# Kernel tuning notes

Hardware: AMD Instinct MI355X
Metric: run time of the kernel (lower is better)

## Reference

```python
import jax, jax.numpy as jnp
from jax import lax
import numpy as np

B, T, TW, EW = 32, 64, 32, 300   # dialogues, utterances, words, word-embed
H = 512                          # lstm hidden per direction
E = 2 * H                        # utterance embedding size
HH = 512                         # emotion hidden size
C = 7                            # output classes


def setup_inputs() -> dict:
    key = jax.random.key(0)
    ks = jax.random.split(key, 24)
    n = lambda k, shp: (jax.random.normal(k, shp, dtype=jnp.float32) * 0.05)
    inp = {
        "input_data": jax.random.normal(ks[0], (B, T, TW, EW), dtype=jnp.float32),
        # BiLSTM (torch gate order i,f,g,o)
        "lstm_Wih_f": n(ks[1], (4 * H, EW)), "lstm_Whh_f": n(ks[2], (4 * H, H)), "lstm_b_f": n(ks[3], (4 * H,)),
        "lstm_Wih_b": n(ks[4], (4 * H, EW)), "lstm_Whh_b": n(ks[5], (4 * H, H)), "lstm_b_b": n(ks[6], (4 * H,)),
        # attention weight
        "W_att": n(ks[7], (E, E)),
        # global-state GRUCell (torch gate order r,z,n)
        "g_Wih": n(ks[8], (3 * E, E)), "g_Whh": n(ks[9], (3 * E, E)), "g_bih": n(ks[10], (3 * E,)), "g_bhh": n(ks[11], (3 * E,)),
        # party-state GRUCell
        "p_Wih": n(ks[12], (3 * E, E)), "p_Whh": n(ks[13], (3 * E, E)), "p_bih": n(ks[14], (3 * E,)), "p_bhh": n(ks[15], (3 * E,)),
        # emotion-state GRUCell (input E, hidden HH)
        "e_Wih": n(ks[16], (3 * HH, E)), "e_Whh": n(ks[17], (3 * HH, HH)), "e_bih": n(ks[18], (3 * HH,)), "e_bhh": n(ks[19], (3 * HH,)),
        # classifier
        "cls_W": n(ks[20], (C, HH)), "cls_b": n(ks[21], (C,)),
    }
    return inp


def _gru_cell(x, h, Wih, Whh, bih, bhh):
    gi = x @ Wih.T + bih
    gh = h @ Whh.T + bhh
    ir, iz, inn = jnp.split(gi, 3, axis=-1)
    hr, hz, hn = jnp.split(gh, 3, axis=-1)
    r = jax.nn.sigmoid(ir + hr)
    z = jax.nn.sigmoid(iz + hz)
    n = jnp.tanh(inn + r * hn)
    return (1.0 - z) * n + z * h


def _lstm_last_hidden(xs, Wih, Whh, b):
    # xs: [Tw, N, Ew] -> final hidden [N, H]
    N = xs.shape[1]
    h0 = jnp.zeros((N, H), xs.dtype)

    def step(carry, x):
        h, c = carry
        g = x @ Wih.T + h @ Whh.T + b
        i_, f_, g_, o_ = jnp.split(g, 4, axis=-1)
        c2 = jax.nn.sigmoid(f_) * c + jax.nn.sigmoid(i_) * jnp.tanh(g_)
        h2 = jax.nn.sigmoid(o_) * jnp.tanh(c2)
        return (h2, c2), None

    (h, _), _ = lax.scan(step, (h0, h0), xs)
    return h


def _forward(input_data, lstm_Wih_f, lstm_Whh_f, lstm_b_f, lstm_Wih_b, lstm_Whh_b, lstm_b_b,
             W_att, g_Wih, g_Whh, g_bih, g_bhh, p_Wih, p_Whh, p_bih, p_bhh,
             e_Wih, e_Whh, e_bih, e_bhh, cls_W, cls_b):
    # ---- FeatureExtraction: BiLSTM over words, take fwd-last + bwd-first hidden ----
    x = input_data.reshape(B * T, TW, EW).transpose(1, 0, 2)          # [Tw, N, Ew]
    h_fwd = _lstm_last_hidden(x, lstm_Wih_f, lstm_Whh_f, lstm_b_f)     # [N, H]
    h_bwd = _lstm_last_hidden(x[::-1], lstm_Wih_b, lstm_Whh_b, lstm_b_b)  # [N, H]
    feats = jnp.concatenate([h_fwd, h_bwd], axis=-1).reshape(B, T, E)  # [B, T, 2H]

    # ---- EmotionDetection: sequential recurrence over utterances ----
    utt = feats.transpose(1, 0, 2)                                     # [T, B, E]
    hist0 = jnp.zeros((T + 1, B, E), feats.dtype)   # global_state history (idx 0 = zero init)
    party0 = jnp.zeros((2, B, E), feats.dtype)
    emo0 = jnp.zeros((B, HH), feats.dtype)
    l_idx = jnp.arange(T + 1)[:, None]              # [T+1, 1]

    def step(carry, inp):
        hist, party, emo = carry
        x_i, i = inp
        p = i % 2
        g_prev = hist[i]                                               # global_state[i]
        new_g = _gru_cell(x_i + party[p], g_prev, g_Wih, g_Whh, g_bih, g_bhh)
        hist = hist.at[i + 1].set(new_g)
        # attention over history indices 0..i (excludes the just-appended state)
        q = x_i @ W_att                                                # [B, E]
        scores = jnp.einsum('be,lbe->lb', q, hist)                     # [T+1, B]
        scores = jnp.where(l_idx <= i, scores, -jnp.inf)
        w = jax.nn.softmax(scores, axis=0)[:, :, None]                 # [T+1, B, 1]
        context = jnp.sum(hist * w, axis=0)                            # [B, E]
        new_p = _gru_cell(x_i + context, party[p], p_Wih, p_Whh, p_bih, p_bhh)
        party = party.at[p].set(new_p)
        emo = _gru_cell(new_p, emo, e_Wih, e_Whh, e_bih, e_bhh)        # [B, HH]
        return (hist, party, emo), emo

    _, emo_seq = lax.scan(step, (hist0, party0, emo0), (utt, jnp.arange(T)))
    emo_seq = emo_seq.transpose(1, 0, 2)                               # [B, T, HH]
    return emo_seq @ cls_W.T + cls_b                                   # [B, T, C]


def reference(input_data, lstm_Wih_f, lstm_Whh_f, lstm_b_f, lstm_Wih_b, lstm_Whh_b, lstm_b_b,
              W_att, g_Wih, g_Whh, g_bih, g_bhh, p_Wih, p_Whh, p_bih, p_bhh,
              e_Wih, e_Whh, e_bih, e_bhh, cls_W, cls_b):
    return _forward(input_data, lstm_Wih_f, lstm_Whh_f, lstm_b_f, lstm_Wih_b, lstm_Whh_b, lstm_b_b,
                    W_att, g_Wih, g_Whh, g_bih, g_bhh, p_Wih, p_Whh, p_bih, p_bhh,
                    e_Wih, e_Whh, e_bih, e_bhh, cls_W, cls_b)
```

## Files before the change

kernel.cpp:

```cpp
#include <hip/hip_runtime.h>
#include <math.h>

#define B_  32
#define T_  64
#define TW_ 32
#define EW_ 300
#define H_  512
#define E_  1024
#define HH_ 512
#define C_  7
#define N_  2048

typedef float f32x4 __attribute__((ext_vector_type(4)));
typedef short s16x8 __attribute__((ext_vector_type(8)));
typedef unsigned short u16;
typedef unsigned int u32;

__device__ __forceinline__ float sigm(float x){ return 1.f/(1.f+expf(-x)); }
__device__ __forceinline__ float bf2f(u16 u){
  union{float f; unsigned v;} x; x.v = ((unsigned)u)<<16; return x.f;
}
__device__ __forceinline__ u16 f2bf(float f){
  union{float f; unsigned v;} x; x.f = f;
  unsigned r = x.v + 0x7FFF + ((x.v>>16)&1);
  return (u16)(r>>16);
}
__device__ __forceinline__ void g2lds16(const void* g, void* l){
  __builtin_amdgcn_global_load_lds((const __attribute__((address_space(1))) u32*)g,
                                   (__attribute__((address_space(3))) u32*)l, 16, 0, 0);
}

__global__ __launch_bounds__(256) void k_pack_w(
    const float* __restrict__ Wih_f, const float* __restrict__ Whh_f,
    const float* __restrict__ Wih_b, const float* __restrict__ Whh_b,
    u16* __restrict__ Wpk)
{
  size_t idx = (size_t)blockIdx.x*256 + threadIdx.x;
  if(idx >= (size_t)32*26*4096) return;
  int c   = (int)(idx & 31);
  int row = (int)((idx >> 5) & 127);
  int kc  = (int)((idx >> 12) % 26);
  int pan = (int)(idx / ((size_t)26*4096));
  int dir = pan >> 4, mt = pan & 15;
  int g = row >> 5, ml = row & 31;
  int R = g*512 + mt*32 + ml;
  int k = kc*32 + c;
  const float* Wih = dir ? Wih_b : Wih_f;
  const float* Whh = dir ? Whh_b : Whh_f;
  float v = (k < 320) ? ((k < EW_) ? Wih[(size_t)R*EW_ + k] : 0.f)
                      : Whh[(size_t)R*H_ + (k-320)];
  Wpk[idx] = f2bf(v);
}

__global__ __launch_bounds__(256) void k_pack_x(
    const float* __restrict__ input, u16* __restrict__ xpk)
{
  size_t idx = (size_t)blockIdx.x*256 + threadIdx.x;
  if(idx >= (size_t)32*32*10*2048) return;
  int c   = (int)(idx & 31);
  int row = (int)((idx >> 5) & 63);
  int kc  = (int)((idx >> 11) % 10);
  int q2  = (int)((idx >> 11) / 10);
  int nt  = q2 & 31, wt = q2 >> 5;
  int n = nt*64 + row;
  int k = kc*32 + c;
  float v = (k < EW_) ? input[((size_t)n*TW_ + wt)*EW_ + k] : 0.f;
  xpk[idx] = f2bf(v);
}

__global__ __launch_bounds__(256) void k_f2bf(const float* __restrict__ src,
                                              u16* __restrict__ dst, int n)
{
  int idx = blockIdx.x*256 + threadIdx.x;
  if(idx < n) dst[idx] = f2bf(src[idx]);
}

__global__ __launch_bounds__(256) void k_wattT(const float* __restrict__ W,
                                               u16* __restrict__ dst)
{
  int idx = blockIdx.x*256 + threadIdx.x;
  if(idx >= E_*E_) return;
  int j = idx >> 10, k = idx & 1023;
  dst[idx] = f2bf(W[(size_t)k*E_ + j]);
}

__global__ __launch_bounds__(256, 4) void lstm4(
    const u16* __restrict__ xpk, const u16* __restrict__ Wpk,
    const float* __restrict__ b_f, const float* __restrict__ b_b,
    const u16* __restrict__ hpk_in, u16* __restrict__ hpk_out,
    float* __restrict__ cb, u16* __restrict__ featsbf, int t)
{
  const int panel = blockIdx.x, nt = blockIdx.y;
  const int dir = panel & 1, mt = panel >> 1;
  const int wt = dir ? (TW_-1-t) : t;
  const u16* srcW = Wpk + (size_t)(dir*16+mt)*26*4096;
  const u16* srcX = xpk + (size_t)(wt*32+nt)*10*2048;
  const u16* srcH = hpk_in + (size_t)(dir*32+nt)*16*2048;

  __shared__ __align__(16) u16 As[3][2048];
  __shared__ __align__(16) u16 Bs[3][4096];

  const int tid = threadIdx.x;
  const int w = tid >> 6, l = tid & 63;
  const int lr = l & 15, lh = l >> 4;
  const int wn = w >> 1, wm = w & 1;

  f32x4 acc[2][4];
  #pragma unroll
  for(int a=0;a<2;a++)
    #pragma unroll
    for(int g=0;g<4;g++) acc[a][g] = (f32x4){0.f,0.f,0.f,0.f};

  auto stage = [&](int kc, int b){
    const u16* aB = (kc < 10) ? (srcX + (size_t)kc*2048) : (srcH + (size_t)(kc-10)*2048);
    const u16* bB = srcW + (size_t)kc*4096;
    g2lds16((const char*)aB + w*1024 + l*16,       (char*)&As[b][0] + w*1024);
    g2lds16((const char*)bB + (w*2)*1024 + l*16,   (char*)&Bs[b][0] + (w*2)*1024);
    g2lds16((const char*)bB + (w*2+1)*1024 + l*16, (char*)&Bs[b][0] + (w*2+1)*1024);
  };

  stage(0, 0);
  stage(1, 1);
  #pragma unroll
  for(int kc=0; kc<26; ++kc){
    if(kc < 25) asm volatile("s_waitcnt vmcnt(3)" ::: "memory");
    else        asm volatile("s_waitcnt vmcnt(0)" ::: "memory");
    __builtin_amdgcn_s_barrier();
    __builtin_amdgcn_sched_barrier(0);
    if(kc+2 < 26) stage(kc+2, (kc+2)%3);
    const int cu = kc % 3;
    s16x8 av[2], bv[4];
    #pragma unroll
    for(int nf=0; nf<2; ++nf)
      av[nf] = *(const s16x8*)&As[cu][(wn*32 + nf*16 + lr)*32 + lh*8];
    #pragma unroll
    for(int g=0; g<4; ++g)
      bv[g] = *(const s16x8*)&Bs[cu][(g*32 + wm*16 + lr)*32 + lh*8];
    #pragma unroll
    for(int g=0; g<4; ++g)
      #pragma unroll
      for(int nf=0; nf<2; ++nf)
        acc[nf][g] = __builtin_amdgcn_mfma_f32_16x16x32_bf16(av[nf], bv[g], acc[nf][g], 0,0,0);
  }

  const float* bias = dir ? b_b : b_f;
  const int col = wm*16 + lr;
  const int m = mt*32 + col;
  const float bi = bias[m], bfv = bias[H_+m], bg = bias[2*H_+m], bo = bias[3*H_+m];
  float* cbp = cb + (size_t)dir*N_*H_;
  u16* hop = hpk_out + ((size_t)(dir*32+nt)*16 + mt)*2048;
  const int n0 = nt*64;
  #pragma unroll
  for(int nf=0; nf<2; ++nf){
    #pragma unroll
    for(int r=0; r<4; ++r){
      const int row = wn*32 + nf*16 + lh*4 + r;
      const int n = n0 + row;
      float gi = acc[nf][0][r] + bi;
      float gf = acc[nf][1][r] + bfv;
      float gc = acc[nf][2][r] + bg;
      float go = acc[nf][3][r] + bo;
      float c_old = cbp[(size_t)n*H_ + m];
      float c2 = sigm(gf)*c_old + sigm(gi)*tanhf(gc);
      float h2 = sigm(go)*tanhf(c2);
      cbp[(size_t)n*H_ + m] = c2;
      if(t == TW_-1) featsbf[(size_t)n*E_ + dir*H_ + m] = f2bf(h2);
      else           hop[row*32 + col] = f2bf(h2);
    }
  }
}

__global__ __launch_bounds__(256) void k_qgemm(const u16* __restrict__ featsbf,
                                               const u16* __restrict__ WattT,
                                               float* __restrict__ q)
{
  const int n0 = blockIdx.x*64, j0 = blockIdx.y*64;
  __shared__ __align__(16) u16 As[64*40];
  __shared__ __align__(16) u16 Bs[64*40];
  const int tid = threadIdx.x;
  const int w = tid>>6, l = tid&63, lr = l&15, lk = (l>>4)*8;
  const int arow = tid>>2, ak8 = (tid&3)*8;

  f32x4 acc[4];
  #pragma unroll
  for(int i=0;i<4;i++) acc[i] = (f32x4){0.f,0.f,0.f,0.f};

  for(int kc=0; kc<32; ++kc){
    *(s16x8*)&As[arow*40 + ak8] = *(const s16x8*)&featsbf[(size_t)(n0+arow)*E_ + kc*32 + ak8];
    *(s16x8*)&Bs[arow*40 + ak8] = *(const s16x8*)&WattT[(size_t)(j0+arow)*E_ + kc*32 + ak8];
    __syncthreads();
    s16x8 av = *(const s16x8*)&As[(w*16 + lr)*40 + lk];
    #pragma unroll
    for(int mf=0; mf<4; ++mf){
      s16x8 bv = *(const s16x8*)&Bs[(mf*16 + lr)*40 + lk];
      acc[mf] = __builtin_amdgcn_mfma_f32_16x16x32_bf16(av, bv, acc[mf], 0,0,0);
    }
    __syncthreads();
  }
  #pragma unroll
  for(int mf=0; mf<4; ++mf)
    #pragma unroll
    for(int r=0; r<4; ++r){
      int n = n0 + w*16 + (l>>4)*4 + r;
      q[(size_t)n*E_ + j0 + mf*16 + lr] = acc[mf][r];
    }
}

struct GArg2 {
  const u16* xA; const u16* xB;
  long ldA; long ldB;
  const u16* W; int K;
};

__device__ __forceinline__ void gemm32v2(const GArg2 a, int R, int xt, int ks,
                                         int KS, int z, float* __restrict__ part,
                                         char* smem)
{
  u16* Xs0 = (u16*)smem;
  u16* Xs1 = Xs0 + 32*40;
  u16* Ws0 = Xs1 + 32*40;
  u16* Ws1 = Ws0 + 128*32;
  const int Kc = a.K / KS;
  const int nch = Kc >> 5;
  const int kb0 = ks * Kc;
  const int tid = threadIdx.x;
  const int w = tid>>6, l = tid&63, lr = l&15, lh = l>>4;

  f32x4 a00={0,0,0,0}, a01={0,0,0,0}, a10={0,0,0,0}, a11={0,0,0,0};

  auto issueW = [&](int c, u16* Wb){
    const int kb = kb0 + c*32;
    #pragma unroll
    for(int c2=0;c2<2;++c2){
      const int cc = w*2 + c2;
      const char* g = (const char*)(a.W + (size_t)(xt*128 + cc*16 + (l>>2))*a.K + kb) + (l&3)*16;
      g2lds16(g, (char*)Wb + cc*1024);
    }
  };
  auto loadX = [&](int c, short4* xr){
    const int kb = kb0 + c*32;
    const int row = tid>>3, k4 = (tid&7)*4;
    short4 xv = *(const short4*)&a.xA[(size_t)row*a.ldA + kb + k4];
    if(a.xB){
      short4 yv = *(const short4*)&a.xB[(size_t)row*a.ldB + kb + k4];
      xv.x = (short)f2bf(bf2f((u16)xv.x)+bf2f((u16)yv.x));
      xv.y = (short)f2bf(bf2f((u16)xv.y)+bf2f((u16)yv.y));
      xv.z = (short)f2bf(bf2f((u16)xv.z)+bf2f((u16)yv.z));
      xv.w = (short)f2bf(bf2f((u16)xv.w)+bf2f((u16)yv.w));
    }
    *xr = xv;
  };
  auto writeX = [&](short4 xv, u16* Xb){
    *(short4*)&Xb[(tid>>3)*40 + (tid&7)*4] = xv;
  };

  short4 xr;
  issueW(0, Ws0); loadX(0, &xr); writeX(xr, Xs0);
  __syncthreads();
  for(int c=0;c<nch;++c){
    u16* Xc = (c&1)?Xs1:Xs0; u16* Wc = (c&1)?Ws1:Ws0;
    u16* Xn = (c&1)?Xs0:Xs1; u16* Wn = (c&1)?Ws0:Ws1;
    const bool pre = (c+1 < nch);
    if(pre){ issueW(c+1, Wn); loadX(c+1, &xr); }
    s16x8 av0 = *(const s16x8*)&Xc[lr*40 + lh*8];
    s16x8 av1 = *(const s16x8*)&Xc[(16+lr)*40 + lh*8];
    s16x8 bv0 = *(const s16x8*)&Wc[(w*32 + lr)*32 + lh*8];
    s16x8 bv1 = *(const s16x8*)&Wc[(w*32 + 16 + lr)*32 + lh*8];
    a00 = __builtin_amdgcn_mfma_f32_16x16x32_bf16(av0, bv0, a00, 0,0,0);
    a01 = __builtin_amdgcn_mfma_f32_16x16x32_bf16(av0, bv1, a01, 0,0,0);
    a10 = __builtin_amdgcn_mfma_f32_16x16x32_bf16(av1, bv0, a10, 0,0,0);
    a11 = __builtin_amdgcn_mfma_f32_16x16x32_bf16(av1, bv1, a11, 0,0,0);
    if(pre) writeX(xr, Xn);
    __syncthreads();
  }
  float* dst = part + (size_t)((z*KS + ks)*B_)*R + xt*128 + w*32;
  f32x4 accs[2][2] = {{a00,a01},{a10,a11}};
  #pragma unroll
  for(int nf=0; nf<2; ++nf)
    #pragma unroll
    for(int mf=0; mf<2; ++mf)
      #pragma unroll
      for(int r=0; r<4; ++r){
        int n = nf*16 + lh*4 + r;
        dst[(size_t)n*R + mf*16 + lr] = accs[nf][mf][r];
      }
}

__device__ __forceinline__ void att_body(const float* __restrict__ q,
                                         const u16* __restrict__ histbf,
                                         const u16* __restrict__ featsbf,
                                         u16* __restrict__ xcbf,
                                         int i, int b, char* smem)
{
  float* qs = (float*)smem;
  float* sc = qs + E_;
  const int tid = threadIdx.x;
  *(float4*)&qs[tid*4] = *(const float4*)&q[((size_t)b*T_ + i)*E_ + tid*4];
  __syncthreads();
  const int wv = tid>>6, ln = tid&63;
  for(int L = wv; L <= i; L += 4){
    const u16* hl = histbf + ((size_t)L*B_ + b)*E_;
    float s = 0.f;
    s16x8 h0 = *(const s16x8*)&hl[ln*16];
    s16x8 h1 = *(const s16x8*)&hl[ln*16 + 8];
    #pragma unroll
    for(int j=0;j<8;j++){
      s += qs[ln*16 + j]     * bf2f((u16)h0[j]);
      s += qs[ln*16 + 8 + j] * bf2f((u16)h1[j]);
    }
    #pragma unroll
    for(int off=32; off; off>>=1) s += __shfl_down(s, off);
    if(ln == 0) sc[L] = s;
  }
  __syncthreads();
  if(tid < 64){
    float v  = (tid <= i) ? sc[tid] : -INFINITY;
    float mx = v;
    #pragma unroll
    for(int off=32; off; off>>=1) mx = fmaxf(mx, __shfl_xor(mx, off));
    float ex = (tid <= i) ? expf(v - mx) : 0.f;
    float sm = ex;
    #pragma unroll
    for(int off=32; off; off>>=1) sm += __shfl_xor(sm, off);
    sc[tid] = ex / sm;
  }
  __syncthreads();
  const int e4 = tid*4;
  float c0=0.f, c1=0.f, c2=0.f, c3=0.f;
  for(int L=0; L<=i; ++L){
    float wl = sc[L];
    short4 hv = *(const short4*)&histbf[((size_t)L*B_ + b)*E_ + e4];
    c0 += wl*bf2f((u16)hv.x);
    c1 += wl*bf2f((u16)hv.y);
    c2 += wl*bf2f((u16)hv.z);
    c3 += wl*bf2f((u16)hv.w);
  }
  const u16* xi = featsbf + ((size_t)b*T_ + i)*E_ + e4;
  xcbf[(size_t)b*E_ + e4 + 0] = f2bf(bf2f(xi[0]) + c0);
  xcbf[(size_t)b*E_ + e4 + 1] = f2bf(bf2f(xi[1]) + c1);
  xcbf[(size_t)b*E_ + e4 + 2] = f2bf(bf2f(xi[2]) + c2);
  xcbf[(size_t)b*E_ + e4 + 3] = f2bf(bf2f(xi[3]) + c3);
}

__device__ __forceinline__ void gru_comb(const float* __restrict__ part, int R, int J, int KS,
                                         const float* __restrict__ bih, const float* __restrict__ bhh,
                                         const float* __restrict__ hprev_f,
                                         float* __restrict__ dst_f,
                                         u16* __restrict__ dstbf,
                                         float* __restrict__ dst_seq, int idx)
{
  const int b = idx / J, e = idx - b*J;
  float ir=0.f, iz=0.f, in_=0.f, hr=0.f, hz=0.f, hn=0.f;
  for(int ks=0; ks<KS; ++ks){
    const float* p0 = part + (size_t)(ks*B_ + b)*R;
    const float* p1 = part + (size_t)((KS+ks)*B_ + b)*R;
    ir += p0[e]; iz += p0[J+e]; in_ += p0[2*J+e];
    hr += p1[e]; hz += p1[J+e]; hn  += p1[2*J+e];
  }
  ir += bih[e]; iz += bih[J+e]; in_ += bih[2*J+e];
  hr += bhh[e]; hz += bhh[J+e]; hn  += bhh[2*J+e];
  const float r = sigm(ir + hr);
  const float z = sigm(iz + hz);
  const float n = tanhf(in_ + r*hn);
  const float hp = hprev_f[(size_t)b*J + e];
  const float h2 = (1.f - z)*n + z*hp;
  dst_f[(size_t)b*J + e] = h2;
  dstbf[(size_t)b*J + e] = f2bf(h2);
  if(dst_seq) dst_seq[(size_t)b*J + e] = h2;
}

__global__ __launch_bounds__(256) void k_A(GArg2 g0, GArg2 g1, GArg2 e0, GArg2 e1,
    float* __restrict__ part_g, float* __restrict__ part_e,
    const float* __restrict__ q, const u16* __restrict__ histbf,
    const u16* __restrict__ featsbf, u16* __restrict__ xcbf, int i)
{
  __shared__ __align__(16) char smem[21504];
  const int x = blockIdx.x;
  if(x < 384){
    if(i >= T_) return;
    const int xt = x % 24, ks = (x/24) & 7, z = x/192;
    gemm32v2(z ? g1 : g0, 3*E_, xt, ks, 8, z, part_g, smem);
  } else if(x < 576){
    if(i < 1) return;
    const int ix = x-384, xt = ix % 12, ks = (ix/12) & 7, z = ix/96;
    gemm32v2(z ? e1 : e0, 3*HH_, xt, ks, 8, z, part_e, smem);
  } else {
    if(i >= T_) return;
    att_body(q, histbf, featsbf, xcbf, i, x-576, smem);
  }
}

__global__ __launch_bounds__(256) void k_B(GArg2 p0, GArg2 p1,
    const float* __restrict__ part_g, const float* __restrict__ part_e,
    const float* __restrict__ g_bih, const float* __restrict__ g_bhh,
    const float* __restrict__ e_bih, const float* __restrict__ e_bhh,
    const float* __restrict__ gf_prev, float* __restrict__ gf_next,
    u16* __restrict__ histbf,
    float* __restrict__ emof, u16* __restrict__ emobf,
    float* __restrict__ emo_seq, float* __restrict__ part_p, int i)
{
  __shared__ __align__(16) char smem[21504];
  const int x = blockIdx.x;
  if(x < 128){
    if(i >= T_) return;
    gru_comb(part_g, 3*E_, E_, 8, g_bih, g_bhh,
             gf_prev, gf_next, histbf + (size_t)(i+1)*B_*E_, nullptr,
             x*256 + (int)threadIdx.x);
  } else if(x < 512){
    if(i >= T_) return;
    const int ix = x-128, xt = ix % 24, ks = (ix/24) & 7, z = ix/192;
    gemm32v2(z ? p1 : p0, 3*E_, xt, ks, 8, z, part_p, smem);
  } else {
    if(i < 1) return;
    gru_comb(part_e, 3*HH_, HH_, 8, e_bih, e_bhh,
             emof, emof, emobf, emo_seq + (size_t)(i-1)*B_*HH_,
             (x-512)*256 + (int)threadIdx.x);
  }
}

__global__ __launch_bounds__(256) void k_C(const float* __restrict__ part_p,
    const float* __restrict__ p_bih, const float* __restrict__ p_bhh,
    float* __restrict__ partyf_p, u16* __restrict__ partybf_p)
{
  const int idx = blockIdx.x*256 + threadIdx.x;
  gru_comb(part_p, 3*E_, E_, 8, p_bih, p_bhh, partyf_p, partyf_p, partybf_p, nullptr, idx);
}

__global__ __launch_bounds__(256) void classify(const float* __restrict__ emo_seq,
    const float* __restrict__ clsW, const float* __restrict__ clsb, float* __restrict__ out)
{
  const int idx = blockIdx.x*256 + threadIdx.x;
  if(idx >= B_*T_*C_) return;
  const int c = idx % C_;
  const int bt = idx / C_;
  const int t = bt % T_, b = bt / T_;
  const float* e = emo_seq + (size_t)(t*B_ + b)*HH_;
  const float* w = clsW + (size_t)c*HH_;
  float s = clsb[c];
  for(int h=0; h<HH_; ++h) s += e[h]*w[h];
  out[idx] = s;
}

extern "C" void kernel_launch(void* const* d_in, const int* in_sizes, int n_in,
                              void* d_out, int out_size, void* d_ws, size_t ws_size,
                              hipStream_t stream)
{
  const float* input  = (const float*)d_in[0];
  const float* Wih_f  = (const float*)d_in[1];
  const float* Whh_f  = (const float*)d_in[2];
  const float* b_f    = (const float*)d_in[3];
  const float* Wih_b  = (const float*)d_in[4];
  const float* Whh_b  = (const float*)d_in[5];
  const float* b_b    = (const float*)d_in[6];
  const float* W_att  = (const float*)d_in[7];
  const float* g_Wih  = (const float*)d_in[8];
  const float* g_Whh  = (const float*)d_in[9];
  const float* g_bih  = (const float*)d_in[10];
  const float* g_bhh  = (const float*)d_in[11];
  const float* p_Wih  = (const float*)d_in[12];
  const float* p_Whh  = (const float*)d_in[13];
  const float* p_bih  = (const float*)d_in[14];
  const float* p_bhh  = (const float*)d_in[15];
  const float* e_Wih  = (const float*)d_in[16];
  const float* e_Whh  = (const float*)d_in[17];
  const float* e_bih  = (const float*)d_in[18];
  const float* e_bhh  = (const float*)d_in[19];
  const float* cls_W  = (const float*)d_in[20];
  const float* cls_b  = (const float*)d_in[21];

  char* base = (char*)d_ws;
  size_t off = 0;
  auto alloc = [&](size_t bytes)->char*{
    char* p = base + off; off += (bytes + 255) & ~(size_t)255; return p;
  };
  u16*   Wpk     = (u16*)alloc((size_t)32*26*4096*2);
  u16*   xpk     = (u16*)alloc((size_t)32*32*10*2048*2);
  u16*   hpkA    = (u16*)alloc((size_t)2*32*16*2048*2);
  u16*   hpkB    = (u16*)alloc((size_t)2*32*16*2048*2);
  float* cb      = (float*)alloc((size_t)2*N_*H_*4);
  u16*   featsbf = (u16*)alloc((size_t)N_*E_*2);
  u16*   eWih    = (u16*)alloc((size_t)3*HH_*E_*2);
  u16*   eWhh    = (u16*)alloc((size_t)3*HH_*HH_*2);
  u16*   histbf  = (u16*)alloc((size_t)(T_+1)*B_*E_*2);
  float* gfbuf   = (float*)alloc((size_t)2*B_*E_*4);
  float* partyf  = (float*)alloc((size_t)2*B_*E_*4);
  u16*   partybf = (u16*)alloc((size_t)2*B_*E_*2);
  float* emof    = (float*)alloc((size_t)B_*HH_*4);
  u16*   emobf   = (u16*)alloc((size_t)B_*HH_*2);
  float* emo_seq = (float*)alloc((size_t)T_*B_*HH_*4);
  u16*   xcbf    = (u16*)alloc((size_t)B_*E_*2);
  float* part_p  = (float*)alloc((size_t)16*B_*3*E_*4);
  u16*   gWih    = (u16*)((char*)xpk + 0);
  u16*   gWhh    = (u16*)((char*)xpk + 6291456);
  u16*   pWih    = (u16*)((char*)xpk + 12582912);
  u16*   pWhh    = (u16*)((char*)xpk + 18874368);
  float* part_e  = (float*)((char*)xpk + 25165824);
  float* q       = (float*)((char*)xpk + 28311552);
  u16*   WattT   = (u16*)((char*)xpk + 36700160);
  float* part_g  = (float*)hpkA;

  hipMemsetAsync(hpkA,    0, (size_t)2*32*16*2048*2, stream);
  hipMemsetAsync(cb,      0, (size_t)2*N_*H_*4, stream);
  hipMemsetAsync(histbf,  0, (size_t)B_*E_*2, stream);
  hipMemsetAsync(gfbuf,   0, (size_t)B_*E_*4, stream);
  hipMemsetAsync(partyf,  0, (size_t)2*B_*E_*4, stream);
  hipMemsetAsync(partybf, 0, (size_t)2*B_*E_*2, stream);
  hipMemsetAsync(emof,    0, (size_t)B_*HH_*4, stream);
  hipMemsetAsync(emobf,   0, (size_t)B_*HH_*2, stream);

  k_pack_w<<<dim3(((size_t)32*26*4096 + 255)/256), 256, 0, stream>>>(Wih_f, Whh_f, Wih_b, Whh_b, Wpk);
  k_pack_x<<<dim3(((size_t)32*32*10*2048 + 255)/256), 256, 0, stream>>>(input, xpk);

  for(int t=0; t<TW_; ++t){
    u16* hin  = (t & 1) ? hpkB : hpkA;
    u16* hout = (t & 1) ? hpkA : hpkB;
    lstm4<<<dim3(32, 32), 256, 0, stream>>>(xpk, Wpk, b_f, b_b, hin, hout, cb, featsbf, t);
  }

  k_f2bf<<<dim3((3*E_*E_+255)/256), 256, 0, stream>>>(g_Wih, gWih, 3*E_*E_);
  k_f2bf<<<dim3((3*E_*E_+255)/256), 256, 0, stream>>>(g_Whh, gWhh, 3*E_*E_);
  k_f2bf<<<dim3((3*E_*E_+255)/256), 256, 0, stream>>>(p_Wih, pWih, 3*E_*E_);
  k_f2bf<<<dim3((3*E_*E_+255)/256), 256, 0, stream>>>(p_Whh, pWhh, 3*E_*E_);
  k_f2bf<<<dim3((3*HH_*E_+255)/256), 256, 0, stream>>>(e_Wih, eWih, 3*HH_*E_);
  k_f2bf<<<dim3((3*HH_*HH_+255)/256), 256, 0, stream>>>(e_Whh, eWhh, 3*HH_*HH_);
  k_wattT<<<dim3((E_*E_+255)/256), 256, 0, stream>>>(W_att, WattT);

  k_qgemm<<<dim3(32, 16), 256, 0, stream>>>(featsbf, WattT, q);

  for(int i=0; i<=T_; ++i){
    const int p  = i & 1;
    const int pe = (i-1) & 1;
    GArg2 ga0{ featsbf + (size_t)i*E_, partybf + (size_t)p*B_*E_, (long)T_*E_, (long)E_, gWih, E_ };
    GArg2 ga1{ histbf + (size_t)i*B_*E_, nullptr, (long)E_, 0, gWhh, E_ };
    GArg2 ea0{ partybf + (size_t)pe*B_*E_, nullptr, (long)E_, 0, eWih, E_ };
    GArg2 ea1{ emobf, nullptr, (long)HH_, 0, eWhh, HH_ };
    k_A<<<dim3(608), 256, 0, stream>>>(ga0, ga1, ea0, ea1, part_g, part_e,
                                       q, histbf, featsbf, xcbf, i);
    GArg2 pa0{ xcbf, nullptr, (long)E_, 0, pWih, E_ };
    GArg2 pa1{ partybf + (size_t)p*B_*E_, nullptr, (long)E_, 0, pWhh, E_ };
    k_B<<<dim3(576), 256, 0, stream>>>(pa0, pa1, part_g, part_e,
                                       g_bih, g_bhh, e_bih, e_bhh,
                                       gfbuf + (size_t)(i&1)*B_*E_,
                                       gfbuf + (size_t)((i+1)&1)*B_*E_,
                                       histbf, emof, emobf, emo_seq, part_p, i);
    if(i < T_){
      k_C<<<dim3(128), 256, 0, stream>>>(part_p, p_bih, p_bhh,
                                         partyf + (size_t)p*B_*E_,
                                         partybf + (size_t)p*B_*E_);
    }
  }

  classify<<<dim3((B_*T_*C_+255)/256), 256, 0, stream>>>(emo_seq, cls_W, cls_b, (float*)d_out);
}
```

Baseline: 2.618 ms.

## Load LSTM GEMM operands directly to registers and pack cell state by tile

The LSTM step kernel drops its triple-buffered LDS staging and barriers. Each wave now reads its MFMA A and B fragments straight from global memory into registers. The cell-state buffer is also moved to the same tiled layout as the hidden state, so each block reads and writes a contiguous 32x64 tile instead of strided rows. This removes LDS traffic and synchronisation, but loses cross-wave operand sharing: the B and A tiles are read redundantly by several waves, which relies on the cache, and global load latency is no longer hidden by explicit prefetch.

```diff
diff --git a/kernel.cpp b/kernel.cpp
--- a/kernel.cpp
+++ b/kernel.cpp
@@ -84,11 +84,11 @@
   dst[idx] = f2bf(W[(size_t)k*E_ + j]);
 }
 
-__global__ __launch_bounds__(256, 4) void lstm4(
+__global__ __launch_bounds__(256, 4) void lstm5(
     const u16* __restrict__ xpk, const u16* __restrict__ Wpk,
     const float* __restrict__ b_f, const float* __restrict__ b_b,
     const u16* __restrict__ hpk_in, u16* __restrict__ hpk_out,
-    float* __restrict__ cb, u16* __restrict__ featsbf, int t)
+    float* __restrict__ cpk, u16* __restrict__ featsbf, int t)
 {
   const int panel = blockIdx.x, nt = blockIdx.y;
   const int dir = panel & 1, mt = panel >> 1;
@@ -97,57 +97,46 @@
   const u16* srcX = xpk + (size_t)(wt*32+nt)*10*2048;
   const u16* srcH = hpk_in + (size_t)(dir*32+nt)*16*2048;
 
-  __shared__ __align__(16) u16 As[3][2048];
-  __shared__ __align__(16) u16 Bs[3][4096];
-
   const int tid = threadIdx.x;
   const int w = tid >> 6, l = tid & 63;
   const int lr = l & 15, lh = l >> 4;
   const int wn = w >> 1, wm = w & 1;
 
+  const int aoff0 = (wn*32 +  0 + lr)*32 + lh*8;
+  const int aoff1 = (wn*32 + 16 + lr)*32 + lh*8;
+  const int boffb = (wm*16 + lr)*32 + lh*8;
+
   f32x4 acc[2][4];
   #pragma unroll
   for(int a=0;a<2;a++)
     #pragma unroll
     for(int g=0;g<4;g++) acc[a][g] = (f32x4){0.f,0.f,0.f,0.f};
 
-  auto stage = [&](int kc, int b){
+  #pragma unroll
+  for(int kc=0; kc<26; ++kc){
     const u16* aB = (kc < 10) ? (srcX + (size_t)kc*2048) : (srcH + (size_t)(kc-10)*2048);
     const u16* bB = srcW + (size_t)kc*4096;
-    g2lds16((const char*)aB + w*1024 + l*16,       (char*)&As[b][0] + w*1024);
-    g2lds16((const char*)bB + (w*2)*1024 + l*16,   (char*)&Bs[b][0] + (w*2)*1024);
-    g2lds16((const char*)bB + (w*2+1)*1024 + l*16, (char*)&Bs[b][0] + (w*2+1)*1024);
-  };
-
-  stage(0, 0);
-  stage(1, 1);
-  #pragma unroll
-  for(int kc=0; kc<26; ++kc){
-    if(kc < 25) asm volatile("s_waitcnt vmcnt(3)" ::: "memory");
-    else        asm volatile("s_waitcnt vmcnt(0)" ::: "memory");
-    __builtin_amdgcn_s_barrier();
-    __builtin_amdgcn_sched_barrier(0);
-    if(kc+2 < 26) stage(kc+2, (kc+2)%3);
-    const int cu = kc % 3;
-    s16x8 av[2], bv[4];
-    #pragma unroll
-    for(int nf=0; nf<2; ++nf)
-      av[nf] = *(const s16x8*)&As[cu][(wn*32 + nf*16 + lr)*32 + lh*8];
-    #pragma unroll
-    for(int g=0; g<4; ++g)
-      bv[g] = *(const s16x8*)&Bs[cu][(g*32 + wm*16 + lr)*32 + lh*8];
-    #pragma unroll
-    for(int g=0; g<4; ++g)
-      #pragma unroll
-      for(int nf=0; nf<2; ++nf)
-        acc[nf][g] = __builtin_amdgcn_mfma_f32_16x16x32_bf16(av[nf], bv[g], acc[nf][g], 0,0,0);
+    s16x8 av0 = *(const s16x8*)&aB[aoff0];
+    s16x8 av1 = *(const s16x8*)&aB[aoff1];
+    s16x8 bv0 = *(const s16x8*)&bB[boffb];
+    s16x8 bv1 = *(const s16x8*)&bB[boffb + 1024];
+    s16x8 bv2 = *(const s16x8*)&bB[boffb + 2048];
+    s16x8 bv3 = *(const s16x8*)&bB[boffb + 3072];
+    acc[0][0] = __builtin_amdgcn_mfma_f32_16x16x32_bf16(av0, bv0, acc[0][0], 0,0,0);
+    acc[0][1] = __builtin_amdgcn_mfma_f32_16x16x32_bf16(av0, bv1, acc[0][1], 0,0,0);
+    acc[0][2] = __builtin_amdgcn_mfma_f32_16x16x32_bf16(av0, bv2, acc[0][2], 0,0,0);
+    acc[0][3] = __builtin_amdgcn_mfma_f32_16x16x32_bf16(av0, bv3, acc[0][3], 0,0,0);
+    acc[1][0] = __builtin_amdgcn_mfma_f32_16x16x32_bf16(av1, bv0, acc[1][0], 0,0,0);
+    acc[1][1] = __builtin_amdgcn_mfma_f32_16x16x32_bf16(av1, bv1, acc[1][1], 0,0,0);
+    acc[1][2] = __builtin_amdgcn_mfma_f32_16x16x32_bf16(av1, bv2, acc[1][2], 0,0,0);
+    acc[1][3] = __builtin_amdgcn_mfma_f32_16x16x32_bf16(av1, bv3, acc[1][3], 0,0,0);
   }
 
   const float* bias = dir ? b_b : b_f;
   const int col = wm*16 + lr;
   const int m = mt*32 + col;
   const float bi = bias[m], bfv = bias[H_+m], bg = bias[2*H_+m], bo = bias[3*H_+m];
-  float* cbp = cb + (size_t)dir*N_*H_;
+  float* cp = cpk + ((size_t)(dir*32+nt)*16 + mt)*2048;
   u16* hop = hpk_out + ((size_t)(dir*32+nt)*16 + mt)*2048;
   const int n0 = nt*64;
   #pragma unroll
@@ -155,16 +144,15 @@
     #pragma unroll
     for(int r=0; r<4; ++r){
       const int row = wn*32 + nf*16 + lh*4 + r;
-      const int n = n0 + row;
       float gi = acc[nf][0][r] + bi;
       float gf = acc[nf][1][r] + bfv;
       float gc = acc[nf][2][r] + bg;
       float go = acc[nf][3][r] + bo;
-      float c_old = cbp[(size_t)n*H_ + m];
+      float c_old = cp[row*32 + col];
       float c2 = sigm(gf)*c_old + sigm(gi)*tanhf(gc);
       float h2 = sigm(go)*tanhf(c2);
-      cbp[(size_t)n*H_ + m] = c2;
-      if(t == TW_-1) featsbf[(size_t)n*E_ + dir*H_ + m] = f2bf(h2);
+      cp[row*32 + col] = c2;
+      if(t == TW_-1) featsbf[(size_t)(n0+row)*E_ + dir*H_ + m] = f2bf(h2);
       else           hop[row*32 + col] = f2bf(h2);
     }
   }
@@ -477,7 +465,7 @@
   u16*   xpk     = (u16*)alloc((size_t)32*32*10*2048*2);
   u16*   hpkA    = (u16*)alloc((size_t)2*32*16*2048*2);
   u16*   hpkB    = (u16*)alloc((size_t)2*32*16*2048*2);
-  float* cb      = (float*)alloc((size_t)2*N_*H_*4);
+  float* cpk     = (float*)alloc((size_t)2*32*16*2048*4);
   u16*   featsbf = (u16*)alloc((size_t)N_*E_*2);
   u16*   eWih    = (u16*)alloc((size_t)3*HH_*E_*2);
   u16*   eWhh    = (u16*)alloc((size_t)3*HH_*HH_*2);
@@ -500,7 +488,7 @@
   float* part_g  = (float*)hpkA;
 
   hipMemsetAsync(hpkA,    0, (size_t)2*32*16*2048*2, stream);
-  hipMemsetAsync(cb,      0, (size_t)2*N_*H_*4, stream);
+  hipMemsetAsync(cpk,     0, (size_t)2*32*16*2048*4, stream);
   hipMemsetAsync(histbf,  0, (size_t)B_*E_*2, stream);
   hipMemsetAsync(gfbuf,   0, (size_t)B_*E_*4, stream);
   hipMemsetAsync(partyf,  0, (size_t)2*B_*E_*4, stream);
@@ -514,7 +502,7 @@
   for(int t=0; t<TW_; ++t){
     u16* hin  = (t & 1) ? hpkB : hpkA;
     u16* hout = (t & 1) ? hpkA : hpkB;
-    lstm4<<<dim3(32, 32), 256, 0, stream>>>(xpk, Wpk, b_f, b_b, hin, hout, cb, featsbf, t);
+    lstm5<<<dim3(32, 32), 256, 0, stream>>>(xpk, Wpk, b_f, b_b, hin, hout, cpk, featsbf, t);
   }
 
   k_f2bf<<<dim3((3*E_*E_+255)/256), 256, 0, stream>>>(g_Wih, gWih, 3*E_*E_);
```

Result: slower. 3.206 ms (+22.4%).

## Shrink LSTM tiles for more blocks and pipeline GRU recurrences into two kernels

Applied to the files above, without the earlier changes.

The LSTM step kernel now uses 16-column M panels instead of 32, which doubles the grid and halves per-block LDS and accumulators. The cell state also moves into a tile-packed layout so each block's accesses are contiguous. The dialogue recurrence is rescheduled into two kernels per step instead of three: party GRU combine and emotion GRU combine are skewed one and two steps behind and merged with the global-state GEMM and attention, while the emotion GEMM moves into the party-GEMM kernel. The goal is fewer launches and serial gaps per step, at the cost of less reuse of A tiles in the LSTM and more complex skewed indexing across steps.

```diff
diff --git a/kernel.cpp b/kernel.cpp
--- a/kernel.cpp
+++ b/kernel.cpp
@@ -33,23 +33,23 @@
 __global__ __launch_bounds__(256) void k_pack_w(
     const float* __restrict__ Wih_f, const float* __restrict__ Whh_f,
     const float* __restrict__ Wih_b, const float* __restrict__ Whh_b,
-    u16* __restrict__ Wpk)
+    u16* __restrict__ Wpk2)
 {
   size_t idx = (size_t)blockIdx.x*256 + threadIdx.x;
-  if(idx >= (size_t)32*26*4096) return;
+  if(idx >= (size_t)64*26*2048) return;
   int c   = (int)(idx & 31);
-  int row = (int)((idx >> 5) & 127);
-  int kc  = (int)((idx >> 12) % 26);
-  int pan = (int)(idx / ((size_t)26*4096));
-  int dir = pan >> 4, mt = pan & 15;
-  int g = row >> 5, ml = row & 31;
-  int R = g*512 + mt*32 + ml;
+  int row = (int)((idx >> 5) & 63);
+  int kc  = (int)((idx >> 11) % 26);
+  int pan = (int)(idx / ((size_t)26*2048));
+  int dir = pan >> 5, ms = pan & 31;
+  int g = row >> 4, ml = row & 15;
+  int R = g*512 + ms*16 + ml;
   int k = kc*32 + c;
   const float* Wih = dir ? Wih_b : Wih_f;
   const float* Whh = dir ? Whh_b : Whh_f;
   float v = (k < 320) ? ((k < EW_) ? Wih[(size_t)R*EW_ + k] : 0.f)
                       : Whh[(size_t)R*H_ + (k-320)];
-  Wpk[idx] = f2bf(v);
+  Wpk2[idx] = f2bf(v);
 }
 
 __global__ __launch_bounds__(256) void k_pack_x(
@@ -84,89 +84,74 @@
   dst[idx] = f2bf(W[(size_t)k*E_ + j]);
 }
 
-__global__ __launch_bounds__(256, 4) void lstm4(
-    const u16* __restrict__ xpk, const u16* __restrict__ Wpk,
+__global__ __launch_bounds__(256, 6) void lstm6(
+    const u16* __restrict__ xpk, const u16* __restrict__ Wpk2,
     const float* __restrict__ b_f, const float* __restrict__ b_b,
     const u16* __restrict__ hpk_in, u16* __restrict__ hpk_out,
-    float* __restrict__ cb, u16* __restrict__ featsbf, int t)
-{
-  const int panel = blockIdx.x, nt = blockIdx.y;
-  const int dir = panel & 1, mt = panel >> 1;
+    float* __restrict__ cpk, u16* __restrict__ featsbf, int t)
+{
+  const int pan = blockIdx.x, nt = blockIdx.y;
+  const int dir = pan & 1, ms = pan >> 1;
   const int wt = dir ? (TW_-1-t) : t;
-  const u16* srcW = Wpk + (size_t)(dir*16+mt)*26*4096;
+  const u16* srcW = Wpk2 + (size_t)(dir*32+ms)*26*2048;
   const u16* srcX = xpk + (size_t)(wt*32+nt)*10*2048;
   const u16* srcH = hpk_in + (size_t)(dir*32+nt)*16*2048;
 
   __shared__ __align__(16) u16 As[3][2048];
-  __shared__ __align__(16) u16 Bs[3][4096];
+  __shared__ __align__(16) u16 Bs[3][2048];
 
   const int tid = threadIdx.x;
   const int w = tid >> 6, l = tid & 63;
   const int lr = l & 15, lh = l >> 4;
-  const int wn = w >> 1, wm = w & 1;
-
-  f32x4 acc[2][4];
+
+  f32x4 acc[4];
   #pragma unroll
-  for(int a=0;a<2;a++)
-    #pragma unroll
-    for(int g=0;g<4;g++) acc[a][g] = (f32x4){0.f,0.f,0.f,0.f};
+  for(int g=0;g<4;g++) acc[g] = (f32x4){0.f,0.f,0.f,0.f};
 
   auto stage = [&](int kc, int b){
     const u16* aB = (kc < 10) ? (srcX + (size_t)kc*2048) : (srcH + (size_t)(kc-10)*2048);
-    const u16* bB = srcW + (size_t)kc*4096;
-    g2lds16((const char*)aB + w*1024 + l*16,       (char*)&As[b][0] + w*1024);
-    g2lds16((const char*)bB + (w*2)*1024 + l*16,   (char*)&Bs[b][0] + (w*2)*1024);
-    g2lds16((const char*)bB + (w*2+1)*1024 + l*16, (char*)&Bs[b][0] + (w*2+1)*1024);
+    const u16* bB = srcW + (size_t)kc*2048;
+    g2lds16((const char*)aB + w*1024 + l*16, (char*)&As[b][0] + w*1024);
+    g2lds16((const char*)bB + w*1024 + l*16, (char*)&Bs[b][0] + w*1024);
   };
 
   stage(0, 0);
   stage(1, 1);
   #pragma unroll
   for(int kc=0; kc<26; ++kc){
-    if(kc < 25) asm volatile("s_waitcnt vmcnt(3)" ::: "memory");
+    if(kc < 25) asm volatile("s_waitcnt vmcnt(2)" ::: "memory");
     else        asm volatile("s_waitcnt vmcnt(0)" ::: "memory");
     __builtin_amdgcn_s_barrier();
     __builtin_amdgcn_sched_barrier(0);
     if(kc+2 < 26) stage(kc+2, (kc+2)%3);
     const int cu = kc % 3;
-    s16x8 av[2], bv[4];
-    #pragma unroll
-    for(int nf=0; nf<2; ++nf)
-      av[nf] = *(const s16x8*)&As[cu][(wn*32 + nf*16 + lr)*32 + lh*8];
-    #pragma unroll
-    for(int g=0; g<4; ++g)
-      bv[g] = *(const s16x8*)&Bs[cu][(g*32 + wm*16 + lr)*32 + lh*8];
-    #pragma unroll
-    for(int g=0; g<4; ++g)
-      #pragma unroll
-      for(int nf=0; nf<2; ++nf)
-        acc[nf][g] = __builtin_amdgcn_mfma_f32_16x16x32_bf16(av[nf], bv[g], acc[nf][g], 0,0,0);
+    s16x8 av = *(const s16x8*)&As[cu][(w*16 + lr)*32 + lh*8];
+    #pragma unroll
+    for(int g=0; g<4; ++g){
+      s16x8 bv = *(const s16x8*)&Bs[cu][(g*16 + lr)*32 + lh*8];
+      acc[g] = __builtin_amdgcn_mfma_f32_16x16x32_bf16(av, bv, acc[g], 0,0,0);
+    }
   }
 
   const float* bias = dir ? b_b : b_f;
-  const int col = wm*16 + lr;
-  const int m = mt*32 + col;
+  const int m = ms*16 + lr;
   const float bi = bias[m], bfv = bias[H_+m], bg = bias[2*H_+m], bo = bias[3*H_+m];
-  float* cbp = cb + (size_t)dir*N_*H_;
-  u16* hop = hpk_out + ((size_t)(dir*32+nt)*16 + mt)*2048;
+  float* cp = cpk + ((size_t)(dir*32+nt)*32 + ms)*1024;
+  u16* hop = hpk_out + ((size_t)(dir*32+nt)*16 + (ms>>1))*2048 + (ms&1)*16;
   const int n0 = nt*64;
   #pragma unroll
-  for(int nf=0; nf<2; ++nf){
-    #pragma unroll
-    for(int r=0; r<4; ++r){
-      const int row = wn*32 + nf*16 + lh*4 + r;
-      const int n = n0 + row;
-      float gi = acc[nf][0][r] + bi;
-      float gf = acc[nf][1][r] + bfv;
-      float gc = acc[nf][2][r] + bg;
-      float go = acc[nf][3][r] + bo;
-      float c_old = cbp[(size_t)n*H_ + m];
-      float c2 = sigm(gf)*c_old + sigm(gi)*tanhf(gc);
-      float h2 = sigm(go)*tanhf(c2);
-      cbp[(size_t)n*H_ + m] = c2;
-      if(t == TW_-1) featsbf[(size_t)n*E_ + dir*H_ + m] = f2bf(h2);
-      else           hop[row*32 + col] = f2bf(h2);
-    }
+  for(int r=0; r<4; ++r){
+    const int row = w*16 + lh*4 + r;
+    float gi = acc[0][r] + bi;
+    float gf = acc[1][r] + bfv;
+    float gc = acc[2][r] + bg;
+    float go = acc[3][r] + bo;
+    float c_old = cp[row*16 + lr];
+    float c2 = sigm(gf)*c_old + sigm(gi)*tanhf(gc);
+    float h2 = sigm(go)*tanhf(c2);
+    cp[row*16 + lr] = c2;
+    if(t == TW_-1) featsbf[(size_t)(n0+row)*E_ + dir*H_ + m] = f2bf(h2);
+    else           hop[row*32 + lr] = f2bf(h2);
   }
 }
 
@@ -369,10 +354,16 @@
   if(dst_seq) dst_seq[(size_t)b*J + e] = h2;
 }
 
-__global__ __launch_bounds__(256) void k_A(GArg2 g0, GArg2 g1, GArg2 e0, GArg2 e1,
-    float* __restrict__ part_g, float* __restrict__ part_e,
+__global__ __launch_bounds__(256) void k_M(GArg2 g0, GArg2 g1,
+    float* __restrict__ part_g,
     const float* __restrict__ q, const u16* __restrict__ histbf,
-    const u16* __restrict__ featsbf, u16* __restrict__ xcbf, int i)
+    const u16* __restrict__ featsbf, u16* __restrict__ xcbf,
+    const float* __restrict__ part_p, const float* __restrict__ p_bih,
+    const float* __restrict__ p_bhh, float* __restrict__ partyf_pm1,
+    u16* __restrict__ partybf_pm1,
+    const float* __restrict__ part_e, const float* __restrict__ e_bih,
+    const float* __restrict__ e_bhh, float* __restrict__ emof,
+    u16* __restrict__ emobf, float* __restrict__ emo_seq, int i)
 {
   __shared__ __align__(16) char smem[21504];
   const int x = blockIdx.x;
@@ -380,50 +371,44 @@
     if(i >= T_) return;
     const int xt = x % 24, ks = (x/24) & 7, z = x/192;
     gemm32v2(z ? g1 : g0, 3*E_, xt, ks, 8, z, part_g, smem);
-  } else if(x < 576){
-    if(i < 1) return;
-    const int ix = x-384, xt = ix % 12, ks = (ix/12) & 7, z = ix/96;
-    gemm32v2(z ? e1 : e0, 3*HH_, xt, ks, 8, z, part_e, smem);
+  } else if(x < 416){
+    if(i >= T_) return;
+    att_body(q, histbf, featsbf, xcbf, i, x-384, smem);
+  } else if(x < 544){
+    const int ip = i-1;
+    if(ip < 0 || ip >= T_) return;
+    gru_comb(part_p, 3*E_, E_, 8, p_bih, p_bhh, partyf_pm1, partyf_pm1,
+             partybf_pm1, nullptr, (x-416)*256 + (int)threadIdx.x);
   } else {
-    if(i >= T_) return;
-    att_body(q, histbf, featsbf, xcbf, i, x-576, smem);
-  }
-}
-
-__global__ __launch_bounds__(256) void k_B(GArg2 p0, GArg2 p1,
-    const float* __restrict__ part_g, const float* __restrict__ part_e,
+    const int ie = i-2;
+    if(ie < 0 || ie >= T_) return;
+    gru_comb(part_e, 3*HH_, HH_, 8, e_bih, e_bhh, emof, emof, emobf,
+             emo_seq + (size_t)ie*B_*HH_, (x-544)*256 + (int)threadIdx.x);
+  }
+}
+
+__global__ __launch_bounds__(256) void k_B2(GArg2 p0, GArg2 p1, GArg2 e0, GArg2 e1,
+    const float* __restrict__ part_g,
     const float* __restrict__ g_bih, const float* __restrict__ g_bhh,
-    const float* __restrict__ e_bih, const float* __restrict__ e_bhh,
     const float* __restrict__ gf_prev, float* __restrict__ gf_next,
     u16* __restrict__ histbf,
-    float* __restrict__ emof, u16* __restrict__ emobf,
-    float* __restrict__ emo_seq, float* __restrict__ part_p, int i)
+    float* __restrict__ part_p, float* __restrict__ part_e, int i)
 {
   __shared__ __align__(16) char smem[21504];
   const int x = blockIdx.x;
   if(x < 128){
     if(i >= T_) return;
-    gru_comb(part_g, 3*E_, E_, 8, g_bih, g_bhh,
-             gf_prev, gf_next, histbf + (size_t)(i+1)*B_*E_, nullptr,
-             x*256 + (int)threadIdx.x);
+    gru_comb(part_g, 3*E_, E_, 8, g_bih, g_bhh, gf_prev, gf_next,
+             histbf + (size_t)(i+1)*B_*E_, nullptr, x*256 + (int)threadIdx.x);
   } else if(x < 512){
     if(i >= T_) return;
     const int ix = x-128, xt = ix % 24, ks = (ix/24) & 7, z = ix/192;
     gemm32v2(z ? p1 : p0, 3*E_, xt, ks, 8, z, part_p, smem);
   } else {
     if(i < 1) return;
-    gru_comb(part_e, 3*HH_, HH_, 8, e_bih, e_bhh,
-             emof, emof, emobf, emo_seq + (size_t)(i-1)*B_*HH_,
-             (x-512)*256 + (int)threadIdx.x);
-  }
-}
-
-__global__ __launch_bounds__(256) void k_C(const float* __restrict__ part_p,
-    const float* __restrict__ p_bih, const float* __restrict__ p_bhh,
-    float* __restrict__ partyf_p, u16* __restrict__ partybf_p)
-{
-  const int idx = blockIdx.x*256 + threadIdx.x;
-  gru_comb(part_p, 3*E_, E_, 8, p_bih, p_bhh, partyf_p, partyf_p, partybf_p, nullptr, idx);
+    const int ix = x-512, xt = ix % 12, ks = (ix/12) & 7, z = ix/96;
+    gemm32v2(z ? e1 : e0, 3*HH_, xt, ks, 8, z, part_e, smem);
+  }
 }
 
 __global__ __launch_bounds__(256) void classify(const float* __restrict__ emo_seq,
@@ -473,11 +458,11 @@
   auto alloc = [&](size_t bytes)->char*{
     char* p = base + off; off += (bytes + 255) & ~(size_t)255; return p;
   };
-  u16*   Wpk     = (u16*)alloc((size_t)32*26*4096*2);
+  u16*   Wpk2    = (u16*)alloc((size_t)64*26*2048*2);
   u16*   xpk     = (u16*)alloc((size_t)32*32*10*2048*2);
   u16*   hpkA    = (u16*)alloc((size_t)2*32*16*2048*2);
   u16*   hpkB    = (u16*)alloc((size_t)2*32*16*2048*2);
-  float* cb      = (float*)alloc((size_t)2*N_*H_*4);
+  float* cpk     = (float*)alloc((size_t)2*32*32*1024*4);
   u16*   featsbf = (u16*)alloc((size_t)N_*E_*2);
   u16*   eWih    = (u16*)alloc((size_t)3*HH_*E_*2);
   u16*   eWhh    = (u16*)alloc((size_t)3*HH_*HH_*2);
@@ -500,7 +485,7 @@
   float* part_g  = (float*)hpkA;
 
   hipMemsetAsync(hpkA,    0, (size_t)2*32*16*2048*2, stream);
-  hipMemsetAsync(cb,      0, (size_t)2*N_*H_*4, stream);
+  hipMemsetAsync(cpk,     0, (size_t)2*32*32*1024*4, stream);
   hipMemsetAsync(histbf,  0, (size_t)B_*E_*2, stream);
   hipMemsetAsync(gfbuf,   0, (size_t)B_*E_*4, stream);
   hipMemsetAsync(partyf,  0, (size_t)2*B_*E_*4, stream);
@@ -508,13 +493,13 @@
   hipMemsetAsync(emof,    0, (size_t)B_*HH_*4, stream);
   hipMemsetAsync(emobf,   0, (size_t)B_*HH_*2, stream);
 
-  k_pack_w<<<dim3(((size_t)32*26*4096 + 255)/256), 256, 0, stream>>>(Wih_f, Whh_f, Wih_b, Whh_b, Wpk);
+  k_pack_w<<<dim3(((size_t)64*26*2048 + 255)/256), 256, 0, stream>>>(Wih_f, Whh_f, Wih_b, Whh_b, Wpk2);
   k_pack_x<<<dim3(((size_t)32*32*10*2048 + 255)/256), 256, 0, stream>>>(input, xpk);
 
   for(int t=0; t<TW_; ++t){
     u16* hin  = (t & 1) ? hpkB : hpkA;
     u16* hout = (t & 1) ? hpkA : hpkB;
-    lstm4<<<dim3(32, 32), 256, 0, stream>>>(xpk, Wpk, b_f, b_b, hin, hout, cb, featsbf, t);
+    lstm6<<<dim3(64, 32), 256, 0, stream>>>(xpk, Wpk2, b_f, b_b, hin, hout, cpk, featsbf, t);
   }
 
   k_f2bf<<<dim3((3*E_*E_+255)/256), 256, 0, stream>>>(g_Wih, gWih, 3*E_*E_);
@@ -527,26 +512,24 @@
 
   k_qgemm<<<dim3(32, 16), 256, 0, stream>>>(featsbf, WattT, q);
 
-  for(int i=0; i<=T_; ++i){
-    const int p  = i & 1;
-    const int pe = (i-1) & 1;
-    GArg2 ga0{ featsbf + (size_t)i*E_, partybf + (size_t)p*B_*E_, (long)T_*E_, (long)E_, gWih, E_ };
+  for(int i=0; i<=T_+1; ++i){
+    GArg2 ga0{ featsbf + (size_t)i*E_, partybf + (size_t)(i&1)*B_*E_, (long)T_*E_, (long)E_, gWih, E_ };
     GArg2 ga1{ histbf + (size_t)i*B_*E_, nullptr, (long)E_, 0, gWhh, E_ };
-    GArg2 ea0{ partybf + (size_t)pe*B_*E_, nullptr, (long)E_, 0, eWih, E_ };
-    GArg2 ea1{ emobf, nullptr, (long)HH_, 0, eWhh, HH_ };
-    k_A<<<dim3(608), 256, 0, stream>>>(ga0, ga1, ea0, ea1, part_g, part_e,
-                                       q, histbf, featsbf, xcbf, i);
-    GArg2 pa0{ xcbf, nullptr, (long)E_, 0, pWih, E_ };
-    GArg2 pa1{ partybf + (size_t)p*B_*E_, nullptr, (long)E_, 0, pWhh, E_ };
-    k_B<<<dim3(576), 256, 0, stream>>>(pa0, pa1, part_g, part_e,
-                                       g_bih, g_bhh, e_bih, e_bhh,
-                                       gfbuf + (size_t)(i&1)*B_*E_,
-                                       gfbuf + (size_t)((i+1)&1)*B_*E_,
-                                       histbf, emof, emobf, emo_seq, part_p, i);
-    if(i < T_){
-      k_C<<<dim3(128), 256, 0, stream>>>(part_p, p_bih, p_bhh,
-                                         partyf + (size_t)p*B_*E_,
-                                         partybf + (size_t)p*B_*E_);
+    k_M<<<dim3(608), 256, 0, stream>>>(ga0, ga1, part_g, q, histbf, featsbf, xcbf,
+                                       part_p, p_bih, p_bhh,
+                                       partyf + (size_t)((i-1)&1)*B_*E_,
+                                       partybf + (size_t)((i-1)&1)*B_*E_,
+                                       part_e, e_bih, e_bhh, emof, emobf, emo_seq, i);
+    if(i <= T_){
+      GArg2 pa0{ xcbf, nullptr, (long)E_, 0, pWih, E_ };
+      GArg2 pa1{ partybf + (size_t)(i&1)*B_*E_, nullptr, (long)E_, 0, pWhh, E_ };
+      GArg2 ea0{ partybf + (size_t)((i-1)&1)*B_*E_, nullptr, (long)E_, 0, eWih, E_ };
+      GArg2 ea1{ emobf, nullptr, (long)HH_, 0, eWhh, HH_ };
+      k_B2<<<dim3(704), 256, 0, stream>>>(pa0, pa1, ea0, ea1, part_g,
+                                          g_bih, g_bhh,
+                                          gfbuf + (size_t)(i&1)*B_*E_,
+                                          gfbuf + (size_t)((i+1)&1)*B_*E_,
+                                          histbf, part_p, part_e, i);
     }
   }
 
```

Result: faster. 2.444 ms (-6.7%).
